# Kernel tuning notes

Measured on AMD Instinct MI355X. Metric: run time of the kernel, lower is better.

## Reference

```python
import jax, jax.numpy as jnp
import numpy as np


def setup_inputs() -> dict:
    key = jax.random.key(0)
    k1, k2 = jax.random.split(key)
    pred = jax.random.normal(k1, (4, 8192, 3), dtype=jnp.float32)
    gt = jax.random.normal(k2, (4, 8192, 3), dtype=jnp.float32)
    return {"pred": pred, "gt": gt}


def reference(pred, gt):
    # pairwise squared distances: [B, N, M]
    diff = pred[:, :, None, :] - gt[:, None, :, :]
    distances = jnp.sum(diff ** 2, axis=-1)
    pred_to_gt = jnp.min(distances, axis=2)  # [B, N]
    gt_to_pred = jnp.min(distances, axis=1)  # [B, M]
    return jnp.mean(pred_to_gt) + jnp.mean(gt_to_pred)
```

## Files before the change

kernel.cpp:

```cpp
#include <hip/hip_runtime.h>
#include <math.h>


typedef _Float16 half8 __attribute__((ext_vector_type(8)));
typedef float f32x16 __attribute__((ext_vector_type(16)));

#define NPTS   8192
#define CLOUD  32768
#define NQ_TOT 65536
#define TT     512
#define NTC    16

#define PT_OFF (256 * 1024)
#define PQ_OFF (256 * 1024 + 2 * 1024 * 1024)

typedef __attribute__((address_space(1))) const unsigned int as1_uint;
typedef __attribute__((address_space(3))) unsigned int as3_uint;

__device__ __forceinline__ void split2(float v, _Float16& h, _Float16& l) {
  h = (_Float16)v; l = (_Float16)(v - (float)h);
}

__device__ __forceinline__ float min_fold(float m, const f32x16& d) {
  float t0 = fminf(fminf(d[0], d[1]), d[2]);
  float t1 = fminf(fminf(d[3], d[4]), d[5]);
  float t2 = fminf(fminf(d[6], d[7]), d[8]);
  float t3 = fminf(fminf(d[9], d[10]), d[11]);
  float t4 = fminf(fminf(d[12], d[13]), d[14]);
  float t5 = fminf(fminf(t0, t1), d[15]);
  float t6 = fminf(fminf(t2, t3), t4);
  return fminf(m, fminf(t5, t6));
}

__global__ __launch_bounds__(256) void pack_points(
    const float* __restrict__ pred, const float* __restrict__ gt,
    half8* __restrict__ pt, half8* __restrict__ pq, float* __restrict__ out) {
  int id = blockIdx.x * 256 + threadIdx.x;
  if (id == 0) out[0] = 0.f;
  int cloud = id >> 15;
  int idx = id & (CLOUD - 1);
  const float* src = cloud ? gt : pred;
  float x = src[3 * idx], y = src[3 * idx + 1], z = src[3 * idx + 2];
  float s = x * x + y * y + z * z;
  _Float16 xh, xl, yh, yl, zh, zl, sh, sl;
  split2(x, xh, xl); split2(y, yh, yl); split2(z, zh, zl); split2(s, sh, sl);
  _Float16 one = (_Float16)1.0f;

  size_t qbase = (size_t)cloud * 65536 + (size_t)idx * 2;
  pq[qbase]     = (half8){xh, xh, xl, xl, yh, yh, yl, yl};
  pq[qbase + 1] = (half8){zh, zh, zl, zl, one, one, sh, sl};

  _Float16 Xh = (_Float16)(-2.f * (float)xh), Xl = (_Float16)(-2.f * (float)xl);
  _Float16 Yh = (_Float16)(-2.f * (float)yh), Yl = (_Float16)(-2.f * (float)yl);
  _Float16 Zh = (_Float16)(-2.f * (float)zh), Zl = (_Float16)(-2.f * (float)zl);
  size_t tbase = (size_t)(cloud ^ 1) * 65536 + (size_t)(idx >> 5) * 64 + (idx & 31);
  pt[tbase]      = (half8){Xh, Xl, Xh, Xl, Yh, Yl, Yh, Yl};
  pt[tbase + 32] = (half8){Zh, Zl, Zh, Zl, sh, sl, one, one};
}

__global__ __launch_bounds__(256, 6) void chamfer_mfma(
    const half8* __restrict__ pt, const half8* __restrict__ pq,
    unsigned int* __restrict__ minbits) {
  __shared__ __align__(16) half8 lds[TT * 2];
  int bid = blockIdx.x;
  int tc   = bid & (NTC - 1);
  int qblk = (bid >> 4) & 31;
  int b    = (bid >> 9) & 3;
  int dir  = bid >> 11;
  int t = threadIdx.x, lane = t & 63, wave = t >> 6;

  const half8* gsrc = pt + (size_t)dir * 65536 + (size_t)b * 16384 + (size_t)tc * 1024;
  #pragma unroll
  for (int i = 0; i < 4; ++i) {
    int seg = i * 4 + wave;
    __builtin_amdgcn_global_load_lds((as1_uint*)(gsrc + seg * 64 + lane),
                                     (as3_uint*)&lds[seg * 64], 16, 0, 0);
  }

  int hi = lane >> 5, ql = lane & 31;
  int qstart = qblk * 256 + wave * 64;
  const half8* pqb = pq + (size_t)dir * 65536 + (size_t)b * 16384 + (size_t)qstart * 2;
  half8 bq0 = pqb[2 * ql + hi];
  half8 bq1 = pqb[2 * (ql + 32) + hi];

  __syncthreads();

  float m0 = INFINITY, m1 = INFINITY;
  f32x16 zero = {};
  #pragma unroll 2
  for (int g = 0; g < TT / 32; ++g) {
    half8 a = lds[g * 64 + lane];
    f32x16 d0 = __builtin_amdgcn_mfma_f32_32x32x16_f16(a, bq0, zero, 0, 0, 0);
    f32x16 d1 = __builtin_amdgcn_mfma_f32_32x32x16_f16(a, bq1, zero, 0, 0, 0);
    m0 = min_fold(m0, d0);
    m1 = min_fold(m1, d1);
  }
  m0 = fminf(m0, __shfl_xor(m0, 32, 64));
  m1 = fminf(m1, __shfl_xor(m1, 32, 64));

  if (lane < 32) {
    size_t qi = (size_t)dir * CLOUD + (size_t)b * NPTS + qstart + ql;
    atomicMin(&minbits[qi],      __float_as_uint(fmaxf(m0, 0.f)));
    atomicMin(&minbits[qi + 32], __float_as_uint(fmaxf(m1, 0.f)));
  }
}

__global__ __launch_bounds__(256) void reduce_kernel(
    const unsigned int* __restrict__ minbits, float* __restrict__ out) {
  __shared__ float wsum[4];
  float acc = 0.f;
  for (int i = blockIdx.x * 256 + threadIdx.x; i < NQ_TOT; i += 64 * 256)
    acc += __uint_as_float(minbits[i]);
  acc *= (1.0f / 32768.0f);
  #pragma unroll
  for (int off = 32; off > 0; off >>= 1) acc += __shfl_down(acc, off, 64);
  int wid = threadIdx.x >> 6;
  if ((threadIdx.x & 63) == 0) wsum[wid] = acc;
  __syncthreads();
  if (threadIdx.x == 0) atomicAdd(out, wsum[0] + wsum[1] + wsum[2] + wsum[3]);
}

extern "C" void kernel_launch(void* const* d_in, const int* in_sizes, int n_in,
                              void* d_out, int out_size, void* d_ws, size_t ws_size,
                              hipStream_t stream) {
  const float* pred = (const float*)d_in[0];
  const float* gt   = (const float*)d_in[1];
  float* out = (float*)d_out;
  unsigned int* minbits = (unsigned int*)d_ws;
  half8* pt = (half8*)((char*)d_ws + PT_OFF);
  half8* pq = (half8*)((char*)d_ws + PQ_OFF);

  pack_points<<<256, 256, 0, stream>>>(pred, gt, pt, pq, out);
  chamfer_mfma<<<4096, 256, 0, stream>>>(pt, pq, minbits);
  reduce_kernel<<<64, 256, 0, stream>>>(minbits, out);
}
```

Measured before the change: 78.40 us.

## Split targets four ways with direct global loads and per-split partial mins

Each block now covers a quarter of the target cloud (2048 points), reading target fragments straight from global memory instead of staging 512-point tiles in LDS, so the grid shrinks from 4096 to 1024 blocks. Atomic min on the workspace is replaced by writing per-split partial minima, which the reduce kernel combines with fminf. The min fold now uses 8 independent accumulators to shorten dependency chains. This removes LDS staging and most atomics, but each wave repeats global/L2 loads of the target data, and occupancy is lower.

After: 81.04 us. +3.4%, slower.

```diff
diff --git a/kernel.cpp b/kernel.cpp
--- a/kernel.cpp
+++ b/kernel.cpp
@@ -7,29 +7,14 @@
 
 #define NPTS   8192
 #define CLOUD  32768
+#define NSPLIT 4
 #define NQ_TOT 65536
-#define TT     512
-#define NTC    16
 
-#define PT_OFF (256 * 1024)
-#define PQ_OFF (256 * 1024 + 2 * 1024 * 1024)
-
-typedef __attribute__((address_space(1))) const unsigned int as1_uint;
-typedef __attribute__((address_space(3))) unsigned int as3_uint;
+#define PT_OFF (1 * 1024 * 1024)
+#define PQ_OFF (3 * 1024 * 1024)
 
 __device__ __forceinline__ void split2(float v, _Float16& h, _Float16& l) {
   h = (_Float16)v; l = (_Float16)(v - (float)h);
-}
-
-__device__ __forceinline__ float min_fold(float m, const f32x16& d) {
-  float t0 = fminf(fminf(d[0], d[1]), d[2]);
-  float t1 = fminf(fminf(d[3], d[4]), d[5]);
-  float t2 = fminf(fminf(d[6], d[7]), d[8]);
-  float t3 = fminf(fminf(d[9], d[10]), d[11]);
-  float t4 = fminf(fminf(d[12], d[13]), d[14]);
-  float t5 = fminf(fminf(t0, t1), d[15]);
-  float t6 = fminf(fminf(t2, t3), t4);
-  return fminf(m, fminf(t5, t6));
 }
 
 __global__ __launch_bounds__(256) void pack_points(
@@ -58,59 +43,69 @@
   pt[tbase + 32] = (half8){Zh, Zl, Zh, Zl, sh, sl, one, one};
 }
 
-__global__ __launch_bounds__(256, 6) void chamfer_mfma(
+__global__ __launch_bounds__(256, 4) void chamfer_mfma(
     const half8* __restrict__ pt, const half8* __restrict__ pq,
-    unsigned int* __restrict__ minbits) {
-  __shared__ __align__(16) half8 lds[TT * 2];
+    float* __restrict__ pmin) {
   int bid = blockIdx.x;
-  int tc   = bid & (NTC - 1);
-  int qblk = (bid >> 4) & 31;
-  int b    = (bid >> 9) & 3;
-  int dir  = bid >> 11;
+  int split = bid & 3;
+  int qblk  = (bid >> 2) & 31;
+  int b     = (bid >> 7) & 3;
+  int dir   = bid >> 9;
   int t = threadIdx.x, lane = t & 63, wave = t >> 6;
+  int hi = lane >> 5, ql = lane & 31;
 
-  const half8* gsrc = pt + (size_t)dir * 65536 + (size_t)b * 16384 + (size_t)tc * 1024;
-  #pragma unroll
-  for (int i = 0; i < 4; ++i) {
-    int seg = i * 4 + wave;
-    __builtin_amdgcn_global_load_lds((as1_uint*)(gsrc + seg * 64 + lane),
-                                     (as3_uint*)&lds[seg * 64], 16, 0, 0);
-  }
-
-  int hi = lane >> 5, ql = lane & 31;
   int qstart = qblk * 256 + wave * 64;
   const half8* pqb = pq + (size_t)dir * 65536 + (size_t)b * 16384 + (size_t)qstart * 2;
   half8 bq0 = pqb[2 * ql + hi];
   half8 bq1 = pqb[2 * (ql + 32) + hi];
 
-  __syncthreads();
+  const half8* ta = pt + (size_t)dir * 65536 + (size_t)b * 16384
+                       + (size_t)split * 4096;
 
-  float m0 = INFINITY, m1 = INFINITY;
+  float vacc0[8], vacc1[8];
+  #pragma unroll
+  for (int j = 0; j < 8; ++j) { vacc0[j] = INFINITY; vacc1[j] = INFINITY; }
+
   f32x16 zero = {};
-  #pragma unroll 2
-  for (int g = 0; g < TT / 32; ++g) {
-    half8 a = lds[g * 64 + lane];
+  #pragma unroll 4
+  for (int g = 0; g < 64; ++g) {
+    half8 a = ta[g * 64 + lane];
     f32x16 d0 = __builtin_amdgcn_mfma_f32_32x32x16_f16(a, bq0, zero, 0, 0, 0);
     f32x16 d1 = __builtin_amdgcn_mfma_f32_32x32x16_f16(a, bq1, zero, 0, 0, 0);
-    m0 = min_fold(m0, d0);
-    m1 = min_fold(m1, d1);
+    #pragma unroll
+    for (int j = 0; j < 8; ++j) {
+      vacc0[j] = fminf(fminf(vacc0[j], d0[2 * j]), d0[2 * j + 1]);
+      vacc1[j] = fminf(fminf(vacc1[j], d1[2 * j]), d1[2 * j + 1]);
+    }
   }
+  float a0 = fminf(fminf(vacc0[0], vacc0[1]), vacc0[2]);
+  float a1 = fminf(fminf(vacc0[3], vacc0[4]), vacc0[5]);
+  float a2 = fminf(vacc0[6], vacc0[7]);
+  float m0 = fminf(fminf(a0, a1), a2);
+  float b0 = fminf(fminf(vacc1[0], vacc1[1]), vacc1[2]);
+  float b1 = fminf(fminf(vacc1[3], vacc1[4]), vacc1[5]);
+  float b2 = fminf(vacc1[6], vacc1[7]);
+  float m1 = fminf(fminf(b0, b1), b2);
   m0 = fminf(m0, __shfl_xor(m0, 32, 64));
   m1 = fminf(m1, __shfl_xor(m1, 32, 64));
 
   if (lane < 32) {
-    size_t qi = (size_t)dir * CLOUD + (size_t)b * NPTS + qstart + ql;
-    atomicMin(&minbits[qi],      __float_as_uint(fmaxf(m0, 0.f)));
-    atomicMin(&minbits[qi + 32], __float_as_uint(fmaxf(m1, 0.f)));
+    size_t qi = (size_t)dir * 32768 + (size_t)b * NPTS + qstart + ql;
+    pmin[(size_t)split * NQ_TOT + qi]      = m0;
+    pmin[(size_t)split * NQ_TOT + qi + 32] = m1;
   }
 }
 
 __global__ __launch_bounds__(256) void reduce_kernel(
-    const unsigned int* __restrict__ minbits, float* __restrict__ out) {
+    const float* __restrict__ pmin, float* __restrict__ out) {
   __shared__ float wsum[4];
   float acc = 0.f;
-  for (int i = blockIdx.x * 256 + threadIdx.x; i < NQ_TOT; i += 64 * 256)
-    acc += __uint_as_float(minbits[i]);
+  for (int i = blockIdx.x * 256 + threadIdx.x; i < NQ_TOT; i += 64 * 256) {
+    float v = pmin[i];
+    #pragma unroll
+    for (int s = 1; s < NSPLIT; ++s) v = fminf(v, pmin[(size_t)s * NQ_TOT + i]);
+    acc += fmaxf(v, 0.f);
+  }
   acc *= (1.0f / 32768.0f);
   #pragma unroll
   for (int off = 32; off > 0; off >>= 1) acc += __shfl_down(acc, off, 64);
@@ -126,11 +121,11 @@
   const float* pred = (const float*)d_in[0];
   const float* gt   = (const float*)d_in[1];
   float* out = (float*)d_out;
-  unsigned int* minbits = (unsigned int*)d_ws;
+  float* pmin = (float*)d_ws;
   half8* pt = (half8*)((char*)d_ws + PT_OFF);
   half8* pq = (half8*)((char*)d_ws + PQ_OFF);
 
   pack_points<<<256, 256, 0, stream>>>(pred, gt, pt, pq, out);
-  chamfer_mfma<<<4096, 256, 0, stream>>>(pt, pq, minbits);
-  reduce_kernel<<<64, 256, 0, stream>>>(minbits, out);
+  chamfer_mfma<<<1024, 256, 0, stream>>>(pt, pq, pmin);
+  reduce_kernel<<<64, 256, 0, stream>>>(pmin, out);
 }
```
